# Kernel optimization log

Hardware: AMD Instinct MI355X
Metric: run time of the kernel (lower is better)

## Reference

```python
import jax, jax.numpy as jnp
from jax import lax
import numpy as np

B, DIM, H, W = 8, 192, 128, 128
HEADS = 4


def setup_inputs() -> dict:
    key = jax.random.key(0)
    k1, k2, k3, k4 = jax.random.split(key, 4)
    x = jax.random.normal(k1, (B, DIM, H, W), dtype=jnp.float32)
    w_qkv = jax.random.normal(k2, (2 * DIM, DIM), dtype=jnp.float32) * 0.05
    w_dw = jax.random.normal(k3, (2 * DIM, 1, 3, 3), dtype=jnp.float32) * 0.1
    w_proj = jax.random.normal(k4, (DIM, DIM), dtype=jnp.float32) * 0.05
    temperature = jnp.ones((HEADS, 1, 1), dtype=jnp.float32)
    return {"x": x, "w_qkv": w_qkv, "w_dw": w_dw, "w_proj": w_proj, "temperature": temperature}


def reference(x, w_qkv, w_dw, w_proj, temperature):
    b, c, h, w = x.shape
    heads = temperature.shape[0]
    head_c = c // heads
    # 1x1 conv: dim -> 2*dim
    qkv = jnp.einsum('oc,bchw->bohw', w_qkv, x)
    # 3x3 depthwise conv over 2*dim channels
    qkv = lax.conv_general_dilated(
        qkv, w_dw, window_strides=(1, 1), padding='SAME',
        feature_group_count=2 * c,
        dimension_numbers=('NCHW', 'OIHW', 'NCHW'))
    q, v = jnp.split(qkv, 2, axis=1)
    # [b, heads, head_c, h*w]
    q = q.reshape(b, heads, head_c, h * w)
    v = v.reshape(b, heads, head_c, h * w)
    # L2-normalize q over spatial dim; k = q
    q = q / jnp.linalg.norm(q, axis=-1, keepdims=True)
    # channel-wise attention: [b, heads, head_c, head_c]
    attn = jnp.einsum('bhcn,bhdn->bhcd', q, q) * temperature[None]
    attn = jax.nn.softmax(attn, axis=-1)
    out = jnp.einsum('bhcd,bhdn->bhcn', attn, v)
    out = out.reshape(b, c, h, w)
    # 1x1 projection
    return jnp.einsum('oc,bchw->bohw', w_proj, out)
```

## Files before the change

### kernel.cpp

```cpp
#include <hip/hip_runtime.h>

#define BB 8
#define CC 192
#define C2 384
#define HH 128
#define WW 128
#define NN 16384
#define NHEADS 4
#define HC 48
#define LTK 196
#define LTK2 98

typedef float f32x4 __attribute__((ext_vector_type(4)));
typedef float f32x16 __attribute__((ext_vector_type(16)));
typedef short s16x4 __attribute__((ext_vector_type(4)));
typedef short s16x8 __attribute__((ext_vector_type(8)));
typedef unsigned short u16;
typedef u16 u16x4 __attribute__((ext_vector_type(4)));
typedef u16 u16x8 __attribute__((ext_vector_type(8)));
typedef unsigned int u32;

__device__ __forceinline__ float bfu2f(u32 u16v) {
  return __uint_as_float(u16v << 16);
}
__device__ __forceinline__ u16 f2bfu(float f) {
  u32 u = __float_as_uint(f);
  return (u16)((u + 0x7fffu + ((u >> 16) & 1u)) >> 16);
}
__device__ __forceinline__ s16x8 ldpair(const u16* p) {
  s16x4 lo = *reinterpret_cast<const s16x4*>(p);
  s16x4 hi = *reinterpret_cast<const s16x4*>(p + 16);
  return __builtin_shufflevector(lo, hi, 0, 1, 2, 3, 4, 5, 6, 7);
}
__device__ __forceinline__ s16x8 ldb64pair(const u32* p) {
  s16x4 lo = *reinterpret_cast<const s16x4*>(p);
  s16x4 hi = *reinterpret_cast<const s16x4*>(p + 2);
  return __builtin_shufflevector(lo, hi, 0, 1, 2, 3, 4, 5, 6, 7);
}

__global__ __launch_bounds__(256) void k0_wcvt(const float* __restrict__ w,
                                               u16* __restrict__ wbf) {
  const int i = (blockIdx.x * 256 + threadIdx.x) * 4;
  f32x4 v = *reinterpret_cast<const f32x4*>(&w[i]);
  u16x4 o;
  o[0] = f2bfu(v[0]); o[1] = f2bfu(v[1]); o[2] = f2bfu(v[2]); o[3] = f2bfu(v[3]);
  *reinterpret_cast<u16x4*>(&wbf[i]) = o;
}

__global__ __launch_bounds__(512, 4) void k1_qkv(
    const float* __restrict__ x, const u16* __restrict__ wbf,
    u16* __restrict__ qkv) {
  const int bx = blockIdx.x;
  const int n0 = (((bx & 7) << 4) + (bx >> 3)) << 7;
  const int b  = blockIdx.y;
  __shared__ u16 Xs[128 * LTK];
  u32* Xsw = reinterpret_cast<u32*>(Xs);
  const int t = threadIdx.x, lane = t & 63;
  const int wid = t >> 6, wo = wid >> 1, wn = wid & 1;
  const int l31 = lane & 31, g2 = lane >> 5;

  {
    const int nq = t & 31, cr = t >> 5;
    const int kpb = cr >> 1;
    const int jh = cr & 1;
    const int prA = 2 * nq + jh;
    const int prB = 64 + 2 * nq + jh;
    const float* xb = x + (size_t)b * CC * NN + n0 + 4 * nq;
    #pragma unroll 6
    for (int i = 0; i < 12; ++i) {
      f32x4 v = *reinterpret_cast<const f32x4*>(xb + (size_t)(cr + 16 * i) * NN);
      u32 A  = (u32)f2bfu(v[0]) | ((u32)f2bfu(v[1]) << 16);
      u32 Bp = (u32)f2bfu(v[2]) | ((u32)f2bfu(v[3]) << 16);
      u32 oA = __shfl_xor(A, 32);
      u32 oB = __shfl_xor(Bp, 32);
      u32 va, vb;
      if (jh) {
        va = (oB & 0xffffu) | (Bp << 16);
        vb = (oB >> 16) | (Bp & 0xffff0000u);
      } else {
        va = (A & 0xffffu) | (oA << 16);
        vb = (A >> 16) | (oA & 0xffff0000u);
      }
      const int col = kpb + 8 * i;
      Xsw[prA * LTK2 + col] = va;
      Xsw[prB * LTK2 + col] = vb;
    }
  }
  __syncthreads();

  const int nb2 = wn * 32;
  const u32* browE = &Xsw[(nb2 + l31) * LTK2 + 4 * g2];
  const u32* browO = &Xsw[(64 + nb2 + l31) * LTK2 + 4 * g2];

  for (int ot = 0; ot < 3; ++ot) {
    const int o0 = ot * 128;
    const u16* wr = wbf + (size_t)(o0 + wo * 32 + l31) * CC + 8 * g2;

    s16x8 afA[6], afB[6];
    #pragma unroll
    for (int s = 0; s < 6; ++s) {
      afA[s] = *reinterpret_cast<const s16x8*>(wr + s * 32);
      afB[s] = *reinterpret_cast<const s16x8*>(wr + s * 32 + 16);
    }

    f32x16 accE, accO;
    #pragma unroll
    for (int e = 0; e < 16; ++e) { accE[e] = 0.f; accO[e] = 0.f; }

    #pragma unroll
    for (int s = 0; s < 6; ++s) {
      s16x8 bfE0 = ldb64pair(browE + 16 * s);
      s16x8 bfE1 = ldb64pair(browE + 16 * s + 8);
      s16x8 bfO0 = ldb64pair(browO + 16 * s);
      s16x8 bfO1 = ldb64pair(browO + 16 * s + 8);
      accE = __builtin_amdgcn_mfma_f32_32x32x16_bf16(afA[s], bfE0, accE, 0, 0, 0);
      accO = __builtin_amdgcn_mfma_f32_32x32x16_bf16(afA[s], bfO0, accO, 0, 0, 0);
      accE = __builtin_amdgcn_mfma_f32_32x32x16_bf16(afB[s], bfE1, accE, 0, 0, 0);
      accO = __builtin_amdgcn_mfma_f32_32x32x16_bf16(afB[s], bfO1, accO, 0, 0, 0);
    }
    #pragma unroll
    for (int r = 0; r < 16; ++r) {
      const int row = (r & 3) + 8 * (r >> 2) + 4 * g2;
      const u32 pk = (u32)f2bfu(accE[r]) | ((u32)f2bfu(accO[r]) << 16);
      *reinterpret_cast<u32*>(
          &qkv[((size_t)b * C2 + o0 + wo * 32 + row) * NN + n0 + wn * 64 + 2 * l31]) = pk;
    }
  }
}

__global__ __launch_bounds__(256) void k2_dw(
    const u16* __restrict__ qkv, const float* __restrict__ wdw,
    u16* __restrict__ out) {
  const int gid = blockIdx.x;
  const int rb = gid & 7;
  const int plane = gid >> 3;
  const int ch = plane % C2;
  const int t = threadIdx.x;
  const int row = rb * 16 + (t >> 4);
  const int x0 = (t & 15) * 8;
  const u16* p = qkv + (size_t)plane * NN;
  const float* wv = wdw + ch * 9;
  float o[8];
  #pragma unroll
  for (int j = 0; j < 8; ++j) o[j] = 0.f;
  #pragma unroll
  for (int dy = 0; dy < 3; ++dy) {
    const int yy = row + dy - 1;
    if ((unsigned)yy < (unsigned)HH) {
      const u16* rp = p + yy * WW;
      u16x8 m = *reinterpret_cast<const u16x8*>(&rp[x0]);
      float px[10];
      px[0] = (x0 > 0) ? bfu2f(rp[x0 - 1]) : 0.f;
      px[9] = (x0 < 120) ? bfu2f(rp[x0 + 8]) : 0.f;
      #pragma unroll
      for (int j = 0; j < 8; ++j) px[j + 1] = bfu2f(m[j]);
      const float w0 = wv[dy * 3 + 0], w1 = wv[dy * 3 + 1], w2 = wv[dy * 3 + 2];
      #pragma unroll
      for (int j = 0; j < 8; ++j)
        o[j] += w0 * px[j] + w1 * px[j + 1] + w2 * px[j + 2];
    }
  }
  u16x8 ov;
  #pragma unroll
  for (int j = 0; j < 8; ++j) ov[j] = f2bfu(o[j]);
  *reinterpret_cast<u16x8*>(&out[(size_t)plane * NN + row * WW + x0]) = ov;
}

__global__ __launch_bounds__(256) void k3_gram(
    const u16* __restrict__ qkvd, float* __restrict__ gpart) {
  const int bh = blockIdx.x, b = bh >> 2, h = bh & 3;
  const int chunk = blockIdx.y;
  const int t = threadIdx.x, lane = t & 63, wv = t >> 6;
  const int l15 = lane & 15, g = lane >> 4;
  __shared__ float red[4][2304];
  const u16* qb = qkvd + ((size_t)b * C2 + h * HC) * NN;

  f32x4 acc[3][3];
  #pragma unroll
  for (int i = 0; i < 3; ++i)
    #pragma unroll
    for (int j = 0; j < 3; ++j)
      #pragma unroll
      for (int e = 0; e < 4; ++e) acc[i][j][e] = 0.f;

  const int nbase = chunk * 1024 + wv * 256;
  #pragma unroll 2
  for (int st = 0; st < 8; ++st) {
    const int n = nbase + st * 32;
    s16x8 cf[3];
    #pragma unroll
    for (int i = 0; i < 3; ++i)
      cf[i] = ldpair(qb + (size_t)(i * 16 + l15) * NN + n + 4 * g);
    #pragma unroll
    for (int i = 0; i < 3; ++i)
      #pragma unroll
      for (int j = 0; j < 3; ++j)
        acc[i][j] = __builtin_amdgcn_mfma_f32_16x16x32_bf16(cf[i], cf[j], acc[i][j], 0, 0, 0);
  }
  #pragma unroll
  for (int i = 0; i < 3; ++i)
    #pragma unroll
    for (int j = 0; j < 3; ++j)
      #pragma unroll
      for (int r = 0; r < 4; ++r)
        red[wv][(i * 16 + 4 * g + r) * 48 + j * 16 + l15] = acc[i][j][r];
  __syncthreads();
  float* gp = gpart + ((size_t)bh * 16 + chunk) * 2304;
  for (int idx = t; idx < 2304; idx += 256)
    gp[idx] = red[0][idx] + red[1][idx] + red[2][idx] + red[3][idx];
}

__global__ __launch_bounds__(256) void k4_soft(
    const float* __restrict__ gpart, const float* __restrict__ temp,
    float* __restrict__ attn) {
  const int bh = blockIdx.x;
  const int h = bh & 3;
  const int t = threadIdx.x;
  __shared__ float G[2304];
  __shared__ float rn[48];
  for (int idx = t; idx < 2304; idx += 256) {
    float s = 0.f;
    #pragma unroll
    for (int c = 0; c < 16; ++c) s += gpart[((size_t)bh * 16 + c) * 2304 + idx];
    G[idx] = s;
  }
  __syncthreads();
  if (t < 48) rn[t] = rsqrtf(G[t * 48 + t]);
  __syncthreads();
  if (t < 48) {
    const float tm = temp[h];
    float v[48];
    float mx = -1e30f;
    #pragma unroll
    for (int j = 0; j < 48; ++j) {
      v[j] = G[t * 48 + j] * rn[t] * rn[j] * tm;
      mx = fmaxf(mx, v[j]);
    }
    float s = 0.f;
    #pragma unroll
    for (int j = 0; j < 48; ++j) { v[j] = expf(v[j] - mx); s += v[j]; }
    const float inv = 1.f / s;
    #pragma unroll
    for (int j = 0; j < 48; ++j)
      attn[(size_t)bh * 2304 + t * 48 + j] = v[j] * inv;
  }
}

__global__ __launch_bounds__(192) void k5_M(
    const float* __restrict__ wproj, const float* __restrict__ attn,
    u16* __restrict__ Mbf) {
  const int o = blockIdx.x;
  const int b = blockIdx.y;
  const int d = threadIdx.x;
  const int h = d / HC, dl = d % HC;
  const float* wrow = wproj + o * CC + h * HC;
  const float* at = attn + ((size_t)(b * NHEADS + h)) * 2304;
  float s = 0.f;
  #pragma unroll
  for (int c = 0; c < HC; ++c) s = fmaf(wrow[c], at[c * HC + dl], s);
  Mbf[((size_t)b * CC + o) * CC + d] = f2bfu(s);
}

__global__ __launch_bounds__(256, 4) void k6_out(
    const u16* __restrict__ Mbf, const u16* __restrict__ qkvd,
    float* __restrict__ out) {
  const int bx = blockIdx.x;
  const int n0 = (((bx & 7) << 4) + (bx >> 3)) << 7;
  const int b  = blockIdx.y;
  __shared__ u16 Vs[128 * LTK];
  u32* Vsw = reinterpret_cast<u32*>(Vs);
  const int t = threadIdx.x, lane = t & 63;
  const int wid = t >> 6, wo = wid >> 1, wn = wid & 1;
  const int l31 = lane & 31, g2 = lane >> 5;

  {
    const int nq = t & 31, cr = t >> 5;
    const int kpb = cr >> 1;
    const int jh = cr & 1;
    const int prA = 2 * nq + jh;
    const int prB = 64 + 2 * nq + jh;
    const u16* vbp = qkvd + ((size_t)b * C2 + CC) * NN + n0 + 4 * nq;
    #pragma unroll 6
    for (int i = 0; i < 24; ++i) {
      u16x4 m = *reinterpret_cast<const u16x4*>(vbp + (size_t)(cr + 8 * i) * NN);
      u32 A  = (u32)m[0] | ((u32)m[1] << 16);
      u32 Bp = (u32)m[2] | ((u32)m[3] << 16);
      u32 oA = __shfl_xor(A, 32);
      u32 oB = __shfl_xor(Bp, 32);
      u32 va, vb;
      if (jh) {
        va = (oB & 0xffffu) | (Bp << 16);
        vb = (oB >> 16) | (Bp & 0xffff0000u);
      } else {
        va = (A & 0xffffu) | (oA << 16);
        vb = (A >> 16) | (oA & 0xffff0000u);
      }
      const int col = kpb + 4 * i;
      Vsw[prA * LTK2 + col] = va;
      Vsw[prB * LTK2 + col] = vb;
    }
  }
  __syncthreads();

  const int nb2 = wn * 32;
  const u32* browE = &Vsw[(nb2 + l31) * LTK2 + 4 * g2];
  const u32* browO = &Vsw[(64 + nb2 + l31) * LTK2 + 4 * g2];
  const u16* Ab = Mbf + (size_t)b * CC * CC;

  for (int ot = 0; ot < 3; ++ot) {
    const int o0 = ot * 64;
    const u16* ar = Ab + (size_t)(o0 + wo * 32 + l31) * CC + 8 * g2;

    s16x8 afA[6], afB[6];
    #pragma unroll
    for (int s = 0; s < 6; ++s) {
      afA[s] = *reinterpret_cast<const s16x8*>(ar + s * 32);
      afB[s] = *reinterpret_cast<const s16x8*>(ar + s * 32 + 16);
    }

    f32x16 accE, accO;
    #pragma unroll
    for (int e = 0; e < 16; ++e) { accE[e] = 0.f; accO[e] = 0.f; }

    #pragma unroll
    for (int s = 0; s < 6; ++s) {
      s16x8 bfE0 = ldb64pair(browE + 16 * s);
      s16x8 bfE1 = ldb64pair(browE + 16 * s + 8);
      s16x8 bfO0 = ldb64pair(browO + 16 * s);
      s16x8 bfO1 = ldb64pair(browO + 16 * s + 8);
      accE = __builtin_amdgcn_mfma_f32_32x32x16_bf16(afA[s], bfE0, accE, 0, 0, 0);
      accO = __builtin_amdgcn_mfma_f32_32x32x16_bf16(afA[s], bfO0, accO, 0, 0, 0);
      accE = __builtin_amdgcn_mfma_f32_32x32x16_bf16(afB[s], bfE1, accE, 0, 0, 0);
      accO = __builtin_amdgcn_mfma_f32_32x32x16_bf16(afB[s], bfO1, accO, 0, 0, 0);
    }
    #pragma unroll
    for (int r = 0; r < 16; ++r) {
      const int row = (r & 3) + 8 * (r >> 2) + 4 * g2;
      float2 st;
      st.x = accE[r];
      st.y = accO[r];
      *reinterpret_cast<float2*>(
          &out[((size_t)b * CC + o0 + wo * 32 + row) * NN + n0 + wn * 64 + 2 * l31]) = st;
    }
  }
}

extern "C" void kernel_launch(void* const* d_in, const int* in_sizes, int n_in,
                              void* d_out, int out_size, void* d_ws, size_t ws_size,
                              hipStream_t stream) {
  const float* x      = (const float*)d_in[0];
  const float* w_qkv  = (const float*)d_in[1];
  const float* w_dw   = (const float*)d_in[2];
  const float* w_proj = (const float*)d_in[3];
  const float* temp   = (const float*)d_in[4];
  float* out = (float*)d_out;

  const size_t OFF_QKV   = 0;
  const size_t OFF_QKVD  = 100663296ULL;
  const size_t OFF_GPART = 201326592ULL;
  const size_t OFF_ATTN  = 206045184ULL;
  const size_t OFF_M     = 206340096ULL;
  const size_t OFF_WBF   = 206929920ULL;
  const size_t NEEDED    = 207077376ULL;
  if (ws_size < NEEDED) return;

  char* ws = (char*)d_ws;
  u16* qkv   = (u16*)(ws + OFF_QKV);
  u16* qkvd  = (u16*)(ws + OFF_QKVD);
  float* gpart = (float*)(ws + OFF_GPART);
  float* attn  = (float*)(ws + OFF_ATTN);
  u16* Mbf   = (u16*)(ws + OFF_M);
  u16* wbf   = (u16*)(ws + OFF_WBF);

  k0_wcvt<<<dim3(72), 256, 0, stream>>>(w_qkv, wbf);
  k1_qkv <<<dim3(128, 8), 512, 0, stream>>>(x, wbf, qkv);
  k2_dw  <<<dim3(BB * C2 * 8), 256, 0, stream>>>(qkv, w_dw, qkvd);
  k3_gram<<<dim3(BB * NHEADS, 16), 256, 0, stream>>>(qkvd, gpart);
  k4_soft<<<dim3(BB * NHEADS), 256, 0, stream>>>(gpart, temp, attn);
  k5_M   <<<dim3(CC, BB), 192, 0, stream>>>(w_proj, attn, Mbf);
  k6_out <<<dim3(128, 8), 256, 0, stream>>>(Mbf, qkvd, out);
}
```

Measured before the change: 214.8 us.

## Fuse V-half depthwise conv into output GEMM kernel, skip storing conv'd V

The depthwise 3x3 conv kernel now processes only the q half of the channels. The v-half conv is recomputed inside the final projection kernel, which writes its results directly into shared memory in the GEMM B-operand layout. This removes the round trip of writing the conv'd V to global memory and reading it back. In exchange the final kernel does more work per block, reads three input rows per tile, stores to LDS with strided scattered 16-bit writes, and lowers the occupancy hint from 4 to 2. Output stores also switch to nontemporal.

```diff
diff --git a/kernel.cpp b/kernel.cpp
--- a/kernel.cpp
+++ b/kernel.cpp
@@ -11,6 +11,7 @@
 #define LTK 196
 #define LTK2 98
 
+typedef float f32x2 __attribute__((ext_vector_type(2)));
 typedef float f32x4 __attribute__((ext_vector_type(4)));
 typedef float f32x16 __attribute__((ext_vector_type(16)));
 typedef short s16x4 __attribute__((ext_vector_type(4)));
@@ -133,12 +134,13 @@
     u16* __restrict__ out) {
   const int gid = blockIdx.x;
   const int rb = gid & 7;
-  const int plane = gid >> 3;
-  const int ch = plane % C2;
+  const int p = gid >> 3;
+  const int b = p / 192, ch = p % 192;
+  const int plane = b * C2 + ch;
   const int t = threadIdx.x;
   const int row = rb * 16 + (t >> 4);
   const int x0 = (t & 15) * 8;
-  const u16* p = qkv + (size_t)plane * NN;
+  const u16* pp = qkv + (size_t)plane * NN;
   const float* wv = wdw + ch * 9;
   float o[8];
   #pragma unroll
@@ -147,7 +149,7 @@
   for (int dy = 0; dy < 3; ++dy) {
     const int yy = row + dy - 1;
     if ((unsigned)yy < (unsigned)HH) {
-      const u16* rp = p + yy * WW;
+      const u16* rp = pp + yy * WW;
       u16x8 m = *reinterpret_cast<const u16x8*>(&rp[x0]);
       float px[10];
       px[0] = (x0 > 0) ? bfu2f(rp[x0 - 1]) : 0.f;
@@ -261,51 +263,58 @@
   Mbf[((size_t)b * CC + o) * CC + d] = f2bfu(s);
 }
 
-__global__ __launch_bounds__(256, 4) void k6_out(
-    const u16* __restrict__ Mbf, const u16* __restrict__ qkvd,
-    float* __restrict__ out) {
+__global__ __launch_bounds__(256, 2) void k26_convout(
+    const u16* __restrict__ qkv, const float* __restrict__ wdw,
+    const u16* __restrict__ Mbf, float* __restrict__ out) {
   const int bx = blockIdx.x;
-  const int n0 = (((bx & 7) << 4) + (bx >> 3)) << 7;
-  const int b  = blockIdx.y;
+  const int y = ((bx & 7) << 4) + (bx >> 3);
+  const int b = blockIdx.y;
   __shared__ u16 Vs[128 * LTK];
-  u32* Vsw = reinterpret_cast<u32*>(Vs);
   const int t = threadIdx.x, lane = t & 63;
   const int wid = t >> 6, wo = wid >> 1, wn = wid & 1;
   const int l31 = lane & 31, g2 = lane >> 5;
 
-  {
-    const int nq = t & 31, cr = t >> 5;
-    const int kpb = cr >> 1;
-    const int jh = cr & 1;
-    const int prA = 2 * nq + jh;
-    const int prB = 64 + 2 * nq + jh;
-    const u16* vbp = qkvd + ((size_t)b * C2 + CC) * NN + n0 + 4 * nq;
-    #pragma unroll 6
-    for (int i = 0; i < 24; ++i) {
-      u16x4 m = *reinterpret_cast<const u16x4*>(vbp + (size_t)(cr + 8 * i) * NN);
-      u32 A  = (u32)m[0] | ((u32)m[1] << 16);
-      u32 Bp = (u32)m[2] | ((u32)m[3] << 16);
-      u32 oA = __shfl_xor(A, 32);
-      u32 oB = __shfl_xor(Bp, 32);
-      u32 va, vb;
-      if (jh) {
-        va = (oB & 0xffffu) | (Bp << 16);
-        vb = (oB >> 16) | (Bp & 0xffff0000u);
-      } else {
-        va = (A & 0xffffu) | (oA << 16);
-        vb = (A >> 16) | (oA & 0xffff0000u);
+  #pragma unroll
+  for (int it = 0; it < 12; ++it) {
+    const int idx = t + 256 * it;
+    const int ch = idx >> 4;
+    const int grp = idx & 15;
+    const int x0 = grp * 8;
+    const u16* pp = qkv + ((size_t)b * C2 + CC + ch) * NN;
+    const float* wv = wdw + (CC + ch) * 9;
+    float o[8];
+    #pragma unroll
+    for (int j = 0; j < 8; ++j) o[j] = 0.f;
+    #pragma unroll
+    for (int dy = 0; dy < 3; ++dy) {
+      const int yy = y + dy - 1;
+      if ((unsigned)yy < (unsigned)HH) {
+        const u16* rp = pp + yy * WW;
+        u16x8 m = *reinterpret_cast<const u16x8*>(&rp[x0]);
+        float px[10];
+        px[0] = (x0 > 0) ? bfu2f(rp[x0 - 1]) : 0.f;
+        px[9] = (x0 < 120) ? bfu2f(rp[x0 + 8]) : 0.f;
+        #pragma unroll
+        for (int j = 0; j < 8; ++j) px[j + 1] = bfu2f(m[j]);
+        const float w0 = wv[dy * 3 + 0], w1 = wv[dy * 3 + 1], w2 = wv[dy * 3 + 2];
+        #pragma unroll
+        for (int j = 0; j < 8; ++j)
+          o[j] += w0 * px[j] + w1 * px[j + 1] + w2 * px[j + 2];
       }
-      const int col = kpb + 4 * i;
-      Vsw[prA * LTK2 + col] = va;
-      Vsw[prB * LTK2 + col] = vb;
-    }
-  }
-  __syncthreads();
-
-  const int nb2 = wn * 32;
-  const u32* browE = &Vsw[(nb2 + l31) * LTK2 + 4 * g2];
-  const u32* browO = &Vsw[(64 + nb2 + l31) * LTK2 + 4 * g2];
+    }
+    #pragma unroll
+    for (int j = 0; j < 8; ++j) {
+      const int n = x0 + j;
+      Vs[((n >> 1) + 64 * (n & 1)) * LTK + ch] = f2bfu(o[j]);
+    }
+  }
+  __syncthreads();
+
+  const u32* Vsw = reinterpret_cast<const u32*>(Vs);
+  const u32* browE = &Vsw[(wn * 32 + l31) * LTK2 + 4 * g2];
+  const u32* browO = &Vsw[(64 + wn * 32 + l31) * LTK2 + 4 * g2];
   const u16* Ab = Mbf + (size_t)b * CC * CC;
+  float* obase = out + (size_t)b * CC * NN + (y << 7);
 
   for (int ot = 0; ot < 3; ++ot) {
     const int o0 = ot * 64;
@@ -336,11 +345,12 @@
     #pragma unroll
     for (int r = 0; r < 16; ++r) {
       const int row = (r & 3) + 8 * (r >> 2) + 4 * g2;
-      float2 st;
-      st.x = accE[r];
-      st.y = accO[r];
-      *reinterpret_cast<float2*>(
-          &out[((size_t)b * CC + o0 + wo * 32 + row) * NN + n0 + wn * 64 + 2 * l31]) = st;
+      f32x2 st;
+      st[0] = accE[r];
+      st[1] = accO[r];
+      f32x2* op = reinterpret_cast<f32x2*>(
+          &obase[(size_t)(o0 + wo * 32 + row) * NN + wn * 64 + 2 * l31]);
+      __builtin_nontemporal_store(st, op);
     }
   }
 }
@@ -374,9 +384,9 @@
 
   k0_wcvt<<<dim3(72), 256, 0, stream>>>(w_qkv, wbf);
   k1_qkv <<<dim3(128, 8), 512, 0, stream>>>(x, wbf, qkv);
-  k2_dw  <<<dim3(BB * C2 * 8), 256, 0, stream>>>(qkv, w_dw, qkvd);
+  k2_dw  <<<dim3(BB * 192 * 8), 256, 0, stream>>>(qkv, w_dw, qkvd);
   k3_gram<<<dim3(BB * NHEADS, 16), 256, 0, stream>>>(qkvd, gpart);
   k4_soft<<<dim3(BB * NHEADS), 256, 0, stream>>>(gpart, temp, attn);
   k5_M   <<<dim3(CC, BB), 192, 0, stream>>>(w_proj, attn, Mbf);
-  k6_out <<<dim3(128, 8), 256, 0, stream>>>(Mbf, qkvd, out);
-}
+  k26_convout<<<dim3(128, 8), 256, 0, stream>>>(qkv, w_dw, Mbf, out);
+}
```

Measured after the change: 214.2 us. Within noise of the previous version (-0.3%).
